# Performance work log

Measured on AMD Instinct MI355X. Metric: run time of the kernel, lower is better.

The kernel has to match this reference:

```python
import jax, jax.numpy as jnp
import numpy as np

H = 16
W = 16
THRESH = 1.0
B = 32

# NOTE: [5.0, 1.0] reproduces the (likely buggy) constant in the original source.
SRC_POINTS = jnp.array([[0.0,0.0],[0.5,0.0],[1.0,0.0],[0.0,0.5],[0.5,0.5],[1.0,0.5],[0.0,1.0],[5.0,1.0],[1.0,1.0]], dtype=jnp.float32)

def _conv(x, w, stride, padding):
    return jax.lax.conv_general_dilated(x, w, (stride, stride), padding, dimension_numbers=('NHWC', 'HWIO', 'NHWC'))

def _tps_u(r):
    return r * r * jnp.log(r + 1e-6)

def _pdist(a, b):
    # a [...,2], b [n,2] -> [..., n] euclidean distances (eps for sqrt-at-0 safety)
    return jnp.sqrt(jnp.sum((a[..., None, :] - b) ** 2, axis=-1) + 1e-12)

def _tps_fit(ctrl, values):
    # cheind/py-thin-plate-spline TPS.fit with reduced=True. ctrl [n,2], values [n] -> theta [n+2]
    n = ctrl.shape[0]
    K = _tps_u(_pdist(ctrl, ctrl))
    P = jnp.concatenate([jnp.ones((n, 1), ctrl.dtype), ctrl], axis=1)
    A = jnp.zeros((n + 3, n + 3), ctrl.dtype)
    A = A.at[:n, :n].set(K).at[:n, n:].set(P).at[n:, :n].set(P.T)
    v = jnp.zeros(n + 3, ctrl.dtype).at[:n].set(values)
    theta = jnp.linalg.solve(A, v)
    return theta[1:]

def _tps_z(pts, ctrl, theta):
    # pts [m,2], theta reduced [n+2] -> [m]
    U = _tps_u(_pdist(pts, ctrl))
    w, a = theta[:-3], theta[-3:]
    w = jnp.concatenate([-jnp.sum(w, keepdims=True), w])
    return U @ w + a[0] + pts[:, 0] * a[1] + pts[:, 1] * a[2]

def _inlier_mask(geo):
    # geo [18] -> mask [H, W, H, W], mask[a_y, a_x, b_y, b_x]
    mv = geo.reshape(9, 2)
    dst = SRC_POINTS + mv
    delta = SRC_POINTS - dst  # c_src - c_dst (tps_theta_from_points)
    th_x = _tps_fit(dst, delta[:, 0])
    th_y = _tps_fit(dst, delta[:, 1])
    xs = jnp.linspace(0.0, 1.0, W)
    ys = jnp.linspace(0.0, 1.0, H)
    gx, gy = jnp.meshgrid(xs, ys)  # [H, W], gx varies along b_x
    pts = jnp.stack([gx.ravel(), gy.ravel()], axis=-1)
    ax = (gx + _tps_z(pts, dst, th_x).reshape(H, W)) * (H - 1)  # grid[...,0]*(map_size[0]-1)
    ay = (gy + _tps_z(pts, dst, th_y).reshape(H, W)) * (W - 1)
    # integer x in [ceil(ax-t), floor(ax+t)] clipped to [0,W-1]  <=>  |x - ax| <= t for x in range
    ix = jnp.arange(W, dtype=ax.dtype)
    iy = jnp.arange(H, dtype=ay.dtype)
    mx = jnp.abs(ix[:, None, None] - ax[None]) <= THRESH  # [W(a_x), H(b_y), W(b_x)]
    my = jnp.abs(iy[:, None, None] - ay[None]) <= THRESH  # [H(a_y), H(b_y), W(b_x)]
    return (my[:, None] & mx[None]).astype(jnp.float32)   # [H, W, H, W]

def _forward(image_A, image_B, W1, W2, W3, W4, Wr1, Wr2, Wd, bd):
    def feat(img):
        x = jax.nn.relu(_conv(img, W1, 2, 'SAME'))   # 256 -> 128
        x = jax.nn.relu(_conv(x, W2, 2, 'SAME'))     # 128 -> 64
        x = jax.nn.relu(_conv(x, W3, 2, 'SAME'))     # 64 -> 32
        x = jax.nn.relu(_conv(x, W4, 2, 'SAME'))     # 32 -> 16
        return x / (jnp.linalg.norm(x, axis=-1, keepdims=True) + 1e-6)  # channelwise l2 norm
    fA = feat(image_A)
    fB = feat(image_B)
    corr = jnp.einsum('bijc,bklc->bijkl', fA, fB)    # [B, H, W, H, W]
    b = corr.shape[0]
    r = corr.reshape(b, H, W, H * W)
    r = jax.nn.relu(_conv(r, Wr1, 1, 'VALID'))       # 16 -> 10
    r = jax.nn.relu(_conv(r, Wr2, 1, 'VALID'))       # 10 -> 6
    geo = r.reshape(b, -1) @ Wd + bd                 # [B, 18]
    # tf.numpy_function blocks gradients -> stop_gradient on the mask path
    masks = jax.lax.stop_gradient(jax.vmap(_inlier_mask)(geo))
    return jnp.sum(corr * masks, axis=(1, 2, 3, 4))  # [B]

def setup_inputs():
    key = jax.random.key(0)
    ks = jax.random.split(key, 10)
    s = 0.05
    return {
        'image_A': jax.random.normal(ks[0], (B, 256, 256, 3), jnp.float32),
        'image_B': jax.random.normal(ks[1], (B, 256, 256, 3), jnp.float32),
        'W1': jax.random.normal(ks[2], (3, 3, 3, 64), jnp.float32) * s,
        'W2': jax.random.normal(ks[3], (3, 3, 64, 128), jnp.float32) * s,
        'W3': jax.random.normal(ks[4], (3, 3, 128, 256), jnp.float32) * s,
        'W4': jax.random.normal(ks[5], (3, 3, 256, 512), jnp.float32) * s,
        'Wr1': jax.random.normal(ks[6], (7, 7, 256, 128), jnp.float32) * s,
        'Wr2': jax.random.normal(ks[7], (5, 5, 128, 64), jnp.float32) * s,
        'Wd': jax.random.normal(ks[8], (2304, 18), jnp.float32) * s,
        'bd': jnp.zeros((18,), jnp.float32),
    }

def reference(image_A, image_B, W1, W2, W3, W4, Wr1, Wr2, Wd, bd):
    return _forward(image_A, image_B, W1, W2, W3, W4, Wr1, Wr2, Wd, bd)
```

## Files before the change

### kernel.cpp

```cpp
#include <hip/hip_runtime.h>
#include <math.h>


typedef __attribute__((ext_vector_type(8))) _Float16 f16x8;
typedef __attribute__((ext_vector_type(4))) float f32x4;

__device__ __forceinline__ unsigned short f2h(float f) {
  return __builtin_bit_cast(unsigned short, (_Float16)f);
}
__device__ __forceinline__ float h2f(unsigned short u) {
  return (float)__builtin_bit_cast(_Float16, u);
}

__global__ __launch_bounds__(256) void wt_single(const float* __restrict__ w,
                                                 unsigned short* __restrict__ wt,
                                                 int K, int C) {
  const int idx = blockIdx.x * 256 + threadIdx.x;
  if (idx < K * C) {
    const int k = idx / C, o = idx % C;
    wt[(size_t)o * K + k] = f2h(w[idx]);
  }
}

__global__ __launch_bounds__(256) void wt1_prep(const float* __restrict__ w,
                                                unsigned short* __restrict__ wt) {
  const int idx = blockIdx.x * 256 + threadIdx.x;
  if (idx < 2048) {
    const int o = idx >> 5, k = idx & 31;
    wt[idx] = (k < 27) ? f2h(w[(size_t)k * 64 + o]) : (unsigned short)0;
  }
}

__global__ __launch_bounds__(256) void conv1_mfma(const float* __restrict__ in,
                                                  const unsigned short* __restrict__ wt1,
                                                  unsigned short* __restrict__ out) {
  const int i = blockIdx.x;
  const int b = blockIdx.y;
  const int tid = threadIdx.x;
  const int lane = tid & 63, wid = tid >> 6;
  const int lrow = lane & 15, quad = lane >> 4;

  __shared__ _Float16 Rows[3][771];

  const float* __restrict__ inb = in + (size_t)b * 196608;
#pragma unroll
  for (int di = 0; di < 3; ++di) {
    const int y = 2 * i + di;
    if (y < 256) {
      const float* __restrict__ row = inb + (size_t)y * 768;
      for (int e = tid; e < 768; e += 256) Rows[di][e] = (_Float16)row[e];
    } else {
      for (int e = tid; e < 768; e += 256) Rows[di][e] = (_Float16)0.f;
    }
    if (tid < 3) Rows[di][768 + tid] = (_Float16)0.f;
  }
  __syncthreads();

  f16x8 bf[4];
#pragma unroll
  for (int ni = 0; ni < 4; ++ni)
    bf[ni] = *(const f16x8*)(wt1 + (ni * 16 + lrow) * 32 + quad * 8);

  f16x8 af[2];
#pragma unroll
  for (int mi = 0; mi < 2; ++mi) {
    const int j = wid * 32 + mi * 16 + lrow;
#pragma unroll
    for (int s = 0; s < 8; ++s) {
      const int k = quad * 8 + s;
      if (k < 27) {
        const int di = k / 9, dj = (k / 3) % 3, c = k % 3;
        af[mi][s] = Rows[di][(2 * j + dj) * 3 + c];
      } else {
        af[mi][s] = (_Float16)0.f;
      }
    }
  }

  f32x4 acc[2][4];
#pragma unroll
  for (int mi = 0; mi < 2; ++mi)
#pragma unroll
    for (int ni = 0; ni < 4; ++ni) {
      const f32x4 z = {0.f, 0.f, 0.f, 0.f};
      acc[mi][ni] = __builtin_amdgcn_mfma_f32_16x16x32_f16(af[mi], bf[ni], z, 0, 0, 0);
    }

  unsigned short* __restrict__ ob = out + (((size_t)b * 128 + i) * 128) * 64;
#pragma unroll
  for (int mi = 0; mi < 2; ++mi)
#pragma unroll
    for (int ni = 0; ni < 4; ++ni)
#pragma unroll
      for (int r = 0; r < 4; ++r) {
        const int j = wid * 32 + mi * 16 + quad * 4 + r;
        const int col = ni * 16 + lrow;
        ob[(size_t)j * 64 + col] = f2h(fmaxf(acc[mi][ni][r], 0.f));
      }
}

template <int BM, int BN, int CIN, int COUT, int KH, int KW, int STRIDE,
          int SAMEPAD, int SPLIT, int SK, int BATB, int OUTF32, int RELU>
__global__ __launch_bounds__(256) void tile_conv(
    const unsigned short* __restrict__ in, const unsigned short* __restrict__ wt,
    unsigned short* __restrict__ outh, float* __restrict__ outf,
    int Hin, int Win, int Hout, int Wout, int aLo, int bLo) {
  constexpr int LDA = 72;
  constexpr int CPT = CIN / 64;
  constexpr int LA = BM / 32;
  constexpr int LB = BN / 32;
  constexpr int KTOT = KH * KW * CIN;
  constexpr int MT = BM / 32;
  constexpr int NT = BN / 32;
  __shared__ _Float16 As[(1 + SPLIT) * BM * LDA];
  __shared__ _Float16 Bs[(1 + SPLIT) * BN * LDA];

  const int t = threadIdx.x;
  const int lane = t & 63, wid = t >> 6;
  const int lrow = lane & 15, quad = lane >> 4;
  const int m0 = blockIdx.x * BM;
  const int n0 = blockIdx.y * BN;

  int pixB[LA], iS[LA], jS[LA], lofA[LA];
#pragma unroll
  for (int i = 0; i < LA; ++i) {
    const int u = t + 256 * i;
    const int r = u >> 3, sl = u & 7;
    const int m = m0 + r;
    const int j = m % Wout;
    const int t2 = m / Wout;
    const int ii = t2 % Hout;
    const int b = t2 / Hout;
    iS[i] = ii * STRIDE;
    jS[i] = j * STRIDE;
    pixB[i] = ((b * Hin + iS[i]) * Win + jS[i]) * CIN + sl * 8;
    lofA[i] = r * LDA + sl * 8;
  }
  const unsigned short* wb = wt;
  if (BATB) wb += (size_t)(m0 / (Hout * Wout)) * COUT * KTOT;
  int bofB[LB], lofB[LB];
#pragma unroll
  for (int i = 0; i < LB; ++i) {
    const int u = t + 256 * i;
    const int r = u >> 3, sl = u & 7;
    bofB[i] = (n0 + r) * KTOT + sl * 8;
    lofB[i] = r * LDA + sl * 8;
  }

  const f16x8 zh = {0, 0, 0, 0, 0, 0, 0, 0};
  f32x4 acc[MT][NT];
#pragma unroll
  for (int mi = 0; mi < MT; ++mi)
#pragma unroll
    for (int ni = 0; ni < NT; ++ni) acc[mi][ni] = {0.f, 0.f, 0.f, 0.f};

  const int mB = (wid >> 1) * (BM / 2);
  const int nB = (wid & 1) * (BN / 2);

  int tap_lo = 0, tap_hi = KH * KW;
  if (SK > 1) {
    tap_lo = (int)blockIdx.z * KH * KW / SK;
    tap_hi = ((int)blockIdx.z + 1) * KH * KW / SK;
  }
  for (int ch = tap_lo * CPT; ch < tap_hi * CPT; ++ch) {
    const int tap = ch / CPT;
    const int c0 = (ch % CPT) * 64;
    const int di = tap / KW, dj = tap % KW;
    const int toff = (di * Win + dj) * CIN + c0;
    const int woff = tap * CIN + c0;
    f16x8 va[LA], vb[LB], va2[LA], vb2[LB];
#pragma unroll
    for (int i = 0; i < LA; ++i) {
      const bool ok = !SAMEPAD || ((iS[i] + di < Hin) && (jS[i] + dj < Win));
      va[i] = ok ? *(const f16x8*)(in + pixB[i] + toff) : zh;
      if (SPLIT) va2[i] = ok ? *(const f16x8*)(in + pixB[i] + toff + aLo) : zh;
    }
#pragma unroll
    for (int i = 0; i < LB; ++i) {
      vb[i] = *(const f16x8*)(wb + bofB[i] + woff);
      if (SPLIT) vb2[i] = *(const f16x8*)(wb + bofB[i] + woff + bLo);
    }
    __syncthreads();
#pragma unroll
    for (int i = 0; i < LA; ++i) {
      *(f16x8*)&As[lofA[i]] = va[i];
      if (SPLIT) *(f16x8*)&As[BM * LDA + lofA[i]] = va2[i];
    }
#pragma unroll
    for (int i = 0; i < LB; ++i) {
      *(f16x8*)&Bs[lofB[i]] = vb[i];
      if (SPLIT) *(f16x8*)&Bs[BN * LDA + lofB[i]] = vb2[i];
    }
    __syncthreads();
#pragma unroll
    for (int ks = 0; ks < 2; ++ks) {
      f16x8 af[MT], bf[NT], al[MT], bl[NT];
#pragma unroll
      for (int mi = 0; mi < MT; ++mi) {
        const int off = (mB + mi * 16 + lrow) * LDA + ks * 32 + quad * 8;
        af[mi] = *(const f16x8*)&As[off];
        if (SPLIT) al[mi] = *(const f16x8*)&As[BM * LDA + off];
      }
#pragma unroll
      for (int ni = 0; ni < NT; ++ni) {
        const int off = (nB + ni * 16 + lrow) * LDA + ks * 32 + quad * 8;
        bf[ni] = *(const f16x8*)&Bs[off];
        if (SPLIT) bl[ni] = *(const f16x8*)&Bs[BN * LDA + off];
      }
#pragma unroll
      for (int mi = 0; mi < MT; ++mi)
#pragma unroll
        for (int ni = 0; ni < NT; ++ni) {
          if (SPLIT) {
            acc[mi][ni] = __builtin_amdgcn_mfma_f32_16x16x32_f16(af[mi], bl[ni],
                                                                 acc[mi][ni], 0, 0, 0);
            acc[mi][ni] = __builtin_amdgcn_mfma_f32_16x16x32_f16(al[mi], bf[ni],
                                                                 acc[mi][ni], 0, 0, 0);
          }
          acc[mi][ni] = __builtin_amdgcn_mfma_f32_16x16x32_f16(af[mi], bf[ni],
                                                               acc[mi][ni], 0, 0, 0);
        }
    }
  }
  const size_t slice =
      (SK > 1) ? (size_t)blockIdx.z * ((size_t)gridDim.x * BM * COUT) : 0;
#pragma unroll
  for (int mi = 0; mi < MT; ++mi)
#pragma unroll
    for (int ni = 0; ni < NT; ++ni)
#pragma unroll
      for (int r = 0; r < 4; ++r) {
        const int row = m0 + mB + mi * 16 + quad * 4 + r;
        const int col = n0 + nB + ni * 16 + lrow;
        const size_t idx = (size_t)row * COUT + col;
        float v = acc[mi][ni][r];
        if (SK > 1) {
          outf[slice + idx] = v;
        } else if (OUTF32) {
          outf[idx] = v;
          outh[idx] = f2h(v);
        } else {
          if (RELU) v = fmaxf(v, 0.f);
          outh[idx] = f2h(v);
        }
      }
}

template <int MT, int NT, int CIN, int COUT, int KH, int KW, int SK>
__global__ __launch_bounds__(256) void gemm_conv(
    const unsigned short* __restrict__ in, const unsigned short* __restrict__ wt,
    float* __restrict__ outf, int Hin, int Win, int Hout, int Wout) {
  const int KTOT = KH * KW * CIN;
  const int lane = threadIdx.x & 63;
  const int wid = threadIdx.x >> 6;
  const int lrow = lane & 15;
  const int quad = lane >> 4;
  const int m0 = (blockIdx.x * 4 + wid) * (16 * MT);
  const int n0 = blockIdx.y * (16 * NT);

  int pix[MT];
#pragma unroll
  for (int mi = 0; mi < MT; ++mi) {
    const int m = m0 + mi * 16 + lrow;
    const int j = m % Wout;
    const int t = m / Wout;
    const int i = t % Hout;
    const int b = t / Hout;
    pix[mi] = (b * Hin + i) * Win + j;
  }
  const unsigned short* brow[NT];
#pragma unroll
  for (int ni = 0; ni < NT; ++ni)
    brow[ni] = wt + (size_t)(n0 + ni * 16 + lrow) * KTOT + quad * 8;

  f32x4 acc[MT][NT];
#pragma unroll
  for (int mi = 0; mi < MT; ++mi)
#pragma unroll
    for (int ni = 0; ni < NT; ++ni) acc[mi][ni] = {0.f, 0.f, 0.f, 0.f};

  const int tap_lo = (int)blockIdx.z * KH * KW / SK;
  const int tap_hi = ((int)blockIdx.z + 1) * KH * KW / SK;
  for (int tap = tap_lo; tap < tap_hi; ++tap) {
    const int di = tap / KW, dj = tap % KW;
    const unsigned short* ap[MT];
#pragma unroll
    for (int mi = 0; mi < MT; ++mi)
      ap[mi] = in + ((size_t)pix[mi] + di * Win + dj) * CIN + quad * 8;
    const int ko = tap * CIN;
#pragma unroll
    for (int c0 = 0; c0 < CIN; c0 += 32) {
      f16x8 ah[MT], bh[NT];
#pragma unroll
      for (int mi = 0; mi < MT; ++mi) ah[mi] = *(const f16x8*)(ap[mi] + c0);
#pragma unroll
      for (int ni = 0; ni < NT; ++ni) bh[ni] = *(const f16x8*)(brow[ni] + ko + c0);
#pragma unroll
      for (int mi = 0; mi < MT; ++mi)
#pragma unroll
        for (int ni = 0; ni < NT; ++ni)
          acc[mi][ni] = __builtin_amdgcn_mfma_f32_16x16x32_f16(ah[mi], bh[ni],
                                                               acc[mi][ni], 0, 0, 0);
    }
  }
  const size_t slice = (size_t)blockIdx.z * ((size_t)gridDim.x * 64 * MT * COUT);
#pragma unroll
  for (int mi = 0; mi < MT; ++mi)
#pragma unroll
    for (int ni = 0; ni < NT; ++ni)
#pragma unroll
      for (int r = 0; r < 4; ++r) {
        const int row = m0 + mi * 16 + quad * 4 + r;
        const int col = n0 + ni * 16 + lrow;
        outf[slice + (size_t)row * COUT + col] = acc[mi][ni][r];
      }
}

__global__ __launch_bounds__(256) void sum_relu_s(const float* __restrict__ p,
                                                  unsigned short* __restrict__ o,
                                                  int n, int parts) {
  const int idx = blockIdx.x * 256 + threadIdx.x;
  if (idx < n) {
    float v = 0.f;
    for (int s = 0; s < parts; ++s) v += p[(size_t)s * n + idx];
    o[idx] = f2h(fmaxf(v, 0.f));
  }
}
__global__ __launch_bounds__(256) void sum_relu_f(const float* __restrict__ p,
                                                  float* __restrict__ o,
                                                  int n, int parts) {
  const int idx = blockIdx.x * 256 + threadIdx.x;
  if (idx < n) {
    float v = 0.f;
    for (int s = 0; s < parts; ++s) v += p[(size_t)s * n + idx];
    o[idx] = fmaxf(v, 0.f);
  }
}

__global__ __launch_bounds__(64) void l2norm_k(const unsigned short* __restrict__ x,
                                               unsigned short* __restrict__ y,
                                               int loOff) {
  const int lane = threadIdx.x;
  const f16x8 v = *(const f16x8*)(x + (size_t)blockIdx.x * 512 + lane * 8);
  float f[8];
  float s = 0.f;
#pragma unroll
  for (int k = 0; k < 8; ++k) {
    f[k] = (float)v[k];
    s += f[k] * f[k];
  }
#pragma unroll
  for (int off = 32; off; off >>= 1) s += __shfl_xor(s, off, 64);
  const float inv = 1.f / (sqrtf(s) + 1e-6f);
  f16x8 vh, vl;
#pragma unroll
  for (int k = 0; k < 8; ++k) {
    const float nv = f[k] * inv;
    const _Float16 hi = (_Float16)nv;
    vh[k] = hi;
    vl[k] = (_Float16)(nv - (float)hi);
  }
  unsigned short* ph = y + (size_t)blockIdx.x * 512 + lane * 8;
  *(f16x8*)ph = vh;
  *(f16x8*)(ph + (size_t)loOff) = vl;
}

__global__ __launch_bounds__(64) void dense_k(const float* __restrict__ r2,
                                              const float* __restrict__ wd,
                                              const float* __restrict__ bd,
                                              float* __restrict__ geo) {
  const int o = blockIdx.x;
  const int b = blockIdx.y;
  const int lane = threadIdx.x;
  const float* __restrict__ rb = r2 + (size_t)b * 2304;
  float s = 0.f;
  for (int k = lane; k < 2304; k += 64) s += rb[k] * wd[(size_t)k * 18 + o];
#pragma unroll
  for (int off = 32; off; off >>= 1) s += __shfl_xor(s, off, 64);
  if (lane == 0) geo[b * 18 + o] = s + bd[o];
}

__device__ __forceinline__ float tps_u(float r) { return r * r * logf(r + 1e-6f); }

__global__ __launch_bounds__(64) void tps_k(const float* __restrict__ geo,
                                            float* __restrict__ axb,
                                            float* __restrict__ ayb) {
  const int b = blockIdx.x;
  const int tid = threadIdx.x;
  __shared__ float M[12][14];
  __shared__ float fel[12];
  __shared__ float dxs[9], dys[9];
  __shared__ float th[2][12];
  __shared__ float sW[2][9];
  __shared__ float sA[2][3];
  __shared__ int sPiv;

  const float srcx[9] = {0.f, 0.5f, 1.f, 0.f, 0.5f, 1.f, 0.f, 5.f, 1.f};
  const float srcy[9] = {0.f, 0.f, 0.f, 0.5f, 0.5f, 0.5f, 1.f, 1.f, 1.f};

  if (tid < 9) {
    const float mx = geo[b * 18 + 2 * tid], my = geo[b * 18 + 2 * tid + 1];
    dxs[tid] = srcx[tid] + mx;
    dys[tid] = srcy[tid] + my;
    M[tid][12] = -mx;
    M[tid][13] = -my;
  } else if (tid < 12) {
    M[tid][12] = 0.f;
    M[tid][13] = 0.f;
  }
  __syncthreads();
  for (int e = tid; e < 81; e += 64) {
    const int p = e / 9, q = e % 9;
    const float ddx = dxs[p] - dxs[q], ddy = dys[p] - dys[q];
    const float r = sqrtf(ddx * ddx + ddy * ddy + 1e-12f);
    M[p][q] = tps_u(r);
  }
  if (tid < 9) {
    M[tid][9] = 1.f;  M[tid][10] = dxs[tid]; M[tid][11] = dys[tid];
    M[9][tid] = 1.f;  M[10][tid] = dxs[tid]; M[11][tid] = dys[tid];
  } else if (tid < 12) {
    M[tid][9] = 0.f; M[tid][10] = 0.f; M[tid][11] = 0.f;
  }
  __syncthreads();

  for (int k = 0; k < 12; ++k) {
    if (tid == 0) {
      int piv = k;
      float best = fabsf(M[k][k]);
      for (int r = k + 1; r < 12; ++r) {
        const float v = fabsf(M[r][k]);
        if (v > best) { best = v; piv = r; }
      }
      sPiv = piv;
    }
    __syncthreads();
    const int piv = sPiv;
    if (piv != k && tid < 14) {
      const float tmp = M[k][tid];
      M[k][tid] = M[piv][tid];
      M[piv][tid] = tmp;
    }
    __syncthreads();
    if (tid > k && tid < 12) fel[tid] = M[tid][k] / M[k][k];
    __syncthreads();
    for (int e = tid; e < (11 - k) * 14; e += 64) {
      const int r = k + 1 + e / 14, cc = e % 14;
      if (cc >= k) M[r][cc] -= fel[r] * M[k][cc];
    }
    __syncthreads();
  }

  const int grp = tid >> 4;
  const int cc = tid & 15;
  for (int k = 11; k >= 0; --k) {
    float prod = 0.f;
    if (grp < 2 && cc > k && cc < 12) prod = M[k][cc] * th[grp][cc];
#pragma unroll
    for (int off = 8; off; off >>= 1) prod += __shfl_xor(prod, off, 16);
    if (grp < 2 && cc == 0) th[grp][k] = (M[k][12 + grp] - prod) / M[k][k];
    __syncthreads();
  }

  if (tid < 2) {
    float sw = 0.f;
    for (int p = 1; p < 9; ++p) {
      sW[tid][p] = th[tid][p];
      sw += th[tid][p];
    }
    sW[tid][0] = -sw;
    sA[tid][0] = th[tid][9];
    sA[tid][1] = th[tid][10];
    sA[tid][2] = th[tid][11];
  }
  __syncthreads();

  for (int p = tid; p < 256; p += 64) {
    const int pi = p >> 4, pj = p & 15;
    const float x = pj * (1.f / 15.f), y = pi * (1.f / 15.f);
    float zx = sA[0][0] + x * sA[0][1] + y * sA[0][2];
    float zy = sA[1][0] + x * sA[1][1] + y * sA[1][2];
#pragma unroll
    for (int c = 0; c < 9; ++c) {
      const float ddx = x - dxs[c], ddy = y - dys[c];
      const float r = sqrtf(ddx * ddx + ddy * ddy + 1e-12f);
      const float u = tps_u(r);
      zx += u * sW[0][c];
      zy += u * sW[1][c];
    }
    axb[b * 256 + p] = (x + zx) * 15.f;
    ayb[b * 256 + p] = (y + zy) * 15.f;
  }
}

__global__ __launch_bounds__(256) void masksum_k(const float* __restrict__ corr,
                                                 const float* __restrict__ axb,
                                                 const float* __restrict__ ayb,
                                                 float* __restrict__ out) {
  const int b = blockIdx.x;
  const int pB = threadIdx.x;
  const float ax = axb[b * 256 + pB];
  const float ay = ayb[b * 256 + pB];
  const float* __restrict__ cb = corr + (size_t)b * 65536;
  float s = 0.f;
  for (int i = 0; i < 16; ++i) {
    if (fabsf((float)i - ay) <= 1.0f) {
      const float* __restrict__ ci = cb + (size_t)i * 16 * 256 + pB;
      for (int j = 0; j < 16; ++j) {
        if (fabsf((float)j - ax) <= 1.0f) s += ci[(size_t)j * 256];
      }
    }
  }
  __shared__ float sm[256];
  sm[pB] = s;
  __syncthreads();
  for (int off = 128; off; off >>= 1) {
    if (pB < off) sm[pB] += sm[pB + off];
    __syncthreads();
  }
  if (pB == 0) out[b] = sm[0];
}

extern "C" void kernel_launch(void* const* d_in, const int* in_sizes, int n_in,
                              void* d_out, int out_size, void* d_ws, size_t ws_size,
                              hipStream_t stream) {
  const float* imgA = (const float*)d_in[0];
  const float* imgB = (const float*)d_in[1];
  const float* W1 = (const float*)d_in[2];
  const float* W2 = (const float*)d_in[3];
  const float* W3 = (const float*)d_in[4];
  const float* W4 = (const float*)d_in[5];
  const float* Wr1 = (const float*)d_in[6];
  const float* Wr2 = (const float*)d_in[7];
  const float* Wd = (const float*)d_in[8];
  const float* bd = (const float*)d_in[9];

  float* ws = (float*)d_ws;
  unsigned short* WT2 = (unsigned short*)(ws + 0);
  unsigned short* WT3 = (unsigned short*)(ws + 36864);
  unsigned short* WT4 = (unsigned short*)(ws + 184320);
  unsigned short* WTr1 = (unsigned short*)(ws + 774144);
  unsigned short* WTr2 = (unsigned short*)(ws + 1576960);
  unsigned short* FEATs = (unsigned short*)(ws + 1679360);
  unsigned short* S2 = (unsigned short*)(ws + 5873664);
  unsigned short* S1 = (unsigned short*)(ws + 14262272);
  unsigned short* S3 = (unsigned short*)(ws + 14262272);
  unsigned short* FEATsp = (unsigned short*)(ws + 5873664);
  float* CORRf = ws + 14262272;
  unsigned short* CORRh = (unsigned short*)(ws + 16359424);
  float* R1p = ws + 17408000;
  unsigned short* R1h = (unsigned short*)(ws + 20275200);
  float* R2p = ws + 20480000;
  float* R2f = ws + 22323200;
  float* GEOb = ws + 22396928;
  float* AXb = ws + 22397504;
  float* AYb = ws + 22405696;
  unsigned short* WT1 = (unsigned short*)(ws + 31039488);

  wt1_prep<<<8, 256, 0, stream>>>(W1, WT1);
  wt_single<<<288, 256, 0, stream>>>(W2, WT2, 576, 128);
  wt_single<<<1152, 256, 0, stream>>>(W3, WT3, 1152, 256);
  wt_single<<<4608, 256, 0, stream>>>(W4, WT4, 2304, 512);
  wt_single<<<6272, 256, 0, stream>>>(Wr1, WTr1, 12544, 128);
  wt_single<<<800, 256, 0, stream>>>(Wr2, WTr2, 3200, 64);

  for (int img = 0; img < 2; ++img) {
    const float* src = img ? imgB : imgA;
    conv1_mfma<<<dim3(128, 32), 256, 0, stream>>>(src, WT1, S1);
    tile_conv<128, 128, 64, 128, 3, 3, 2, 1, 0, 1, 0, 0, 1>
        <<<dim3(1024, 1), 256, 0, stream>>>(S1, WT2, S2, nullptr,
                                            128, 128, 64, 64, 0, 0);
    tile_conv<128, 128, 128, 256, 3, 3, 2, 1, 0, 1, 0, 0, 1>
        <<<dim3(256, 2), 256, 0, stream>>>(S2, WT3, S3, nullptr,
                                           64, 64, 32, 32, 0, 0);
    tile_conv<64, 128, 256, 512, 3, 3, 2, 1, 0, 1, 0, 0, 1>
        <<<dim3(128, 4), 256, 0, stream>>>(S3, WT4, FEATs + (size_t)img * 4194304,
                                           nullptr, 32, 32, 16, 16, 0, 0);
  }

  l2norm_k<<<16384, 64, 0, stream>>>(FEATs, FEATsp, 8388608);
  tile_conv<64, 64, 512, 256, 1, 1, 1, 0, 1, 1, 1, 1, 0>
      <<<dim3(128, 4), 256, 0, stream>>>(FEATsp, FEATsp + 4194304, CORRh, CORRf,
                                         16, 16, 16, 16, 8388608, 8388608);
  tile_conv<64, 128, 256, 128, 7, 7, 1, 0, 0, 7, 0, 0, 0>
      <<<dim3(50, 1, 7), 256, 0, stream>>>(CORRh, WTr1, nullptr, R1p,
                                           16, 16, 10, 10, 0, 0);
  sum_relu_s<<<1600, 256, 0, stream>>>(R1p, R1h, 409600, 7);
  gemm_conv<1, 4, 128, 64, 5, 5, 25>
      <<<dim3(18, 1, 25), 256, 0, stream>>>(R1h, WTr2, R2p, 10, 10, 6, 6);
  sum_relu_f<<<288, 256, 0, stream>>>(R2p, R2f, 73728, 25);
  dense_k<<<dim3(18, 32), 64, 0, stream>>>(R2f, Wd, bd, GEOb);
  tps_k<<<32, 64, 0, stream>>>(GEOb, AXb, AYb);
  masksum_k<<<32, 256, 0, stream>>>(CORRf, AXb, AYb, (float*)d_out);
}
```

Baseline: 498.5 us.

## Double-buffer shared memory in tile_conv to overlap global loads with MFMA

Turns the single LDS tile in the convolution GEMM kernel into a ping-pong pair. The next channel chunk is loaded from global memory into registers before the current chunk's MFMA work and written to the other buffer afterwards, which removes one barrier per iteration. The aim is to hide global load latency behind compute. The cost is twice the LDS footprint, which may lower occupancy.

```diff
diff --git a/kernel.cpp b/kernel.cpp
--- a/kernel.cpp
+++ b/kernel.cpp
@@ -112,8 +112,8 @@
   constexpr int KTOT = KH * KW * CIN;
   constexpr int MT = BM / 32;
   constexpr int NT = BN / 32;
-  __shared__ _Float16 As[(1 + SPLIT) * BM * LDA];
-  __shared__ _Float16 Bs[(1 + SPLIT) * BN * LDA];
+  __shared__ _Float16 As[2][(1 + SPLIT) * BM * LDA];
+  __shared__ _Float16 Bs[2][(1 + SPLIT) * BN * LDA];
 
   const int t = threadIdx.x;
   const int lane = t & 63, wid = t >> 6;
@@ -162,13 +162,16 @@
     tap_lo = (int)blockIdx.z * KH * KW / SK;
     tap_hi = ((int)blockIdx.z + 1) * KH * KW / SK;
   }
-  for (int ch = tap_lo * CPT; ch < tap_hi * CPT; ++ch) {
+  const int ch_lo = tap_lo * CPT, ch_hi = tap_hi * CPT;
+
+  f16x8 va[LA], vb[LB], va2[LA], vb2[LB];
+
+  auto load_ch = [&](int ch) {
     const int tap = ch / CPT;
     const int c0 = (ch % CPT) * 64;
     const int di = tap / KW, dj = tap % KW;
     const int toff = (di * Win + dj) * CIN + c0;
     const int woff = tap * CIN + c0;
-    f16x8 va[LA], vb[LB], va2[LA], vb2[LB];
 #pragma unroll
     for (int i = 0; i < LA; ++i) {
       const bool ok = !SAMEPAD || ((iS[i] + di < Hin) && (jS[i] + dj < Win));
@@ -180,17 +183,26 @@
       vb[i] = *(const f16x8*)(wb + bofB[i] + woff);
       if (SPLIT) vb2[i] = *(const f16x8*)(wb + bofB[i] + woff + bLo);
     }
-    __syncthreads();
+  };
+  auto write_buf = [&](int buf) {
 #pragma unroll
     for (int i = 0; i < LA; ++i) {
-      *(f16x8*)&As[lofA[i]] = va[i];
-      if (SPLIT) *(f16x8*)&As[BM * LDA + lofA[i]] = va2[i];
+      *(f16x8*)&As[buf][lofA[i]] = va[i];
+      if (SPLIT) *(f16x8*)&As[buf][BM * LDA + lofA[i]] = va2[i];
     }
 #pragma unroll
     for (int i = 0; i < LB; ++i) {
-      *(f16x8*)&Bs[lofB[i]] = vb[i];
-      if (SPLIT) *(f16x8*)&Bs[BN * LDA + lofB[i]] = vb2[i];
-    }
+      *(f16x8*)&Bs[buf][lofB[i]] = vb[i];
+      if (SPLIT) *(f16x8*)&Bs[buf][BN * LDA + lofB[i]] = vb2[i];
+    }
+  };
+
+  load_ch(ch_lo);
+  write_buf(0);
+  int cur = 0;
+  for (int ch = ch_lo; ch < ch_hi; ++ch) {
+    const bool hasNext = (ch + 1 < ch_hi);
+    if (hasNext) load_ch(ch + 1);
     __syncthreads();
 #pragma unroll
     for (int ks = 0; ks < 2; ++ks) {
@@ -198,14 +210,14 @@
 #pragma unroll
       for (int mi = 0; mi < MT; ++mi) {
         const int off = (mB + mi * 16 + lrow) * LDA + ks * 32 + quad * 8;
-        af[mi] = *(const f16x8*)&As[off];
-        if (SPLIT) al[mi] = *(const f16x8*)&As[BM * LDA + off];
+        af[mi] = *(const f16x8*)&As[cur][off];
+        if (SPLIT) al[mi] = *(const f16x8*)&As[cur][BM * LDA + off];
       }
 #pragma unroll
       for (int ni = 0; ni < NT; ++ni) {
         const int off = (nB + ni * 16 + lrow) * LDA + ks * 32 + quad * 8;
-        bf[ni] = *(const f16x8*)&Bs[off];
-        if (SPLIT) bl[ni] = *(const f16x8*)&Bs[BN * LDA + off];
+        bf[ni] = *(const f16x8*)&Bs[cur][off];
+        if (SPLIT) bl[ni] = *(const f16x8*)&Bs[cur][BN * LDA + off];
       }
 #pragma unroll
       for (int mi = 0; mi < MT; ++mi)
@@ -221,6 +233,8 @@
                                                                acc[mi][ni], 0, 0, 0);
         }
     }
+    if (hasNext) write_buf(cur ^ 1);
+    cur ^= 1;
   }
   const size_t slice =
       (SK > 1) ? (size_t)blockIdx.z * ((size_t)gridDim.x * BM * COUT) : 0;
```

Result: faster. 473.0 us (-5.1%).
